# Optimization experiments

Hardware: AMD Instinct MI355X
Metric: run time of the kernel (lower is better)

The kernel has to match this reference:

```python
import jax, jax.numpy as jnp
import numpy as np

HEADS = 8
DIM_KEY = 64


def setup_inputs() -> dict:
    key = jax.random.key(0)
    k1, k2, k3 = jax.random.split(key, 3)
    dim, dim_out = 256, 256
    dim_hidden = HEADS * DIM_KEY  # 512
    img = jax.random.normal(k1, (8, dim, 64, 64), dtype=jnp.float32)
    # 1x1 conv weights stored as [out_ch, in_ch]
    w_qkv = jax.random.normal(k2, (3 * dim_hidden, dim), dtype=jnp.float32) * (dim ** -0.5)
    w_out = jax.random.normal(k3, (dim_out, dim_hidden), dtype=jnp.float32) * (dim_hidden ** -0.5)
    b_out = jnp.zeros((dim_out,), dtype=jnp.float32)
    return {"img": img, "w_qkv": w_qkv, "w_out": w_out, "b_out": b_out}


def reference(img, w_qkv, w_out, b_out):
    b, c, x, y = img.shape
    n = x * y
    # 1x1 conv == channel-mixing GEMM
    qkv = jnp.einsum('oc,bcxy->boxy', w_qkv, img)  # [b, 3*h*dk, x, y]
    q, k, v = jnp.split(qkv, 3, axis=1)
    # 'b (h c) x y -> b h c (x y)'
    reshape = lambda t: t.reshape(b, HEADS, DIM_KEY, n)
    q, k, v = reshape(q), reshape(k), reshape(v)
    k = jax.nn.softmax(k, axis=-1)  # softmax over spatial positions
    context = jnp.einsum('bhdn,bhen->bhde', k, v)      # [b, h, dk, dk]
    content = jnp.einsum('bhde,bhdn->bhen', context, q)  # [b, h, dk, n]
    content = content.reshape(b, HEADS * DIM_KEY, x, y)
    out = jnp.einsum('oc,bcxy->boxy', w_out, content) + b_out[None, :, None, None]
    return out
```

## Files before the change

### kernel.cpp

```cpp
#include <hip/hip_runtime.h>
#include <math.h>
#include <stdint.h>


typedef __attribute__((ext_vector_type(8))) short bf16x8;
typedef __attribute__((ext_vector_type(4))) float f32x4;

#define BATCH 8
#define CIN 256
#define NSP 4096
#define HEADS 8
#define DK 64
#define HID 512
#define OC 256
#define NCH 8
#define NT 4

#define VMCNT(n) asm volatile("s_waitcnt vmcnt(" #n ")" ::: "memory")
#define LGKM0()  asm volatile("s_waitcnt lgkmcnt(0)" ::: "memory")

__device__ __forceinline__ void barrier_fence() {
  asm volatile("" ::: "memory");
  __builtin_amdgcn_s_barrier();
  asm volatile("" ::: "memory");
}

__device__ __forceinline__ void gl16(const void* g, void* l) {
  __builtin_amdgcn_global_load_lds(
      (const __attribute__((address_space(1))) unsigned int*)g,
      (__attribute__((address_space(3))) unsigned int*)l, 16, 0, 0);
}

__device__ __forceinline__ short f2bf(float f) {
  union { float f; uint32_t u; } x; x.f = f;
  uint32_t r = x.u + 0x7fffu + ((x.u >> 16) & 1u);
  return (short)(r >> 16);
}

__device__ __forceinline__ unsigned cvt_pk_bf16(float lo, float hi) {
  unsigned r;
  asm("v_cvt_pk_bf16_f32 %0, %1, %2" : "=v"(r) : "v"(lo), "v"(hi));
  return r;
}

__global__ __launch_bounds__(256) void prep(
    const float* __restrict__ img, const float* __restrict__ w_qkv,
    short* __restrict__ imgT, short* __restrict__ wkv, short* __restrict__ wqT)
{
  __shared__ float t[64][65];
  const int bid = blockIdx.x;
  if (bid < 2048) {
    const int ntile = bid & 63, ctile = (bid >> 6) & 3, b = bid >> 8;
    const float* src = img + ((size_t)b * CIN + ctile * 64) * NSP + ntile * 64;
#pragma unroll
    for (int k = 0; k < 4; ++k) {
      int i = threadIdx.x + k * 256;
      int c = i >> 4, n4 = (i & 15) * 4;
      float4 v = *(const float4*)&src[(size_t)c * NSP + n4];
      t[c][n4 + 0] = v.x; t[c][n4 + 1] = v.y; t[c][n4 + 2] = v.z; t[c][n4 + 3] = v.w;
    }
    __syncthreads();
    short* dst = imgT + ((size_t)b * NSP + ntile * 64) * CIN + ctile * 64;
#pragma unroll
    for (int k = 0; k < 4; ++k) {
      int j = threadIdx.x + k * 256;
      int n = j >> 4, c4 = (j & 15) * 4;
      short r[4] = {f2bf(t[c4 + 0][n]), f2bf(t[c4 + 1][n]),
                    f2bf(t[c4 + 2][n]), f2bf(t[c4 + 3][n])};
      *(uint2*)&dst[(size_t)n * CIN + c4] = *(uint2*)r;
    }
  } else if (bid < 2304) {
    int i = (bid - 2048) * 256 + threadIdx.x;
    const float* src = w_qkv + (size_t)HID * CIN;
    float4 v = ((const float4*)src)[i];
    short r[4] = {f2bf(v.x), f2bf(v.y), f2bf(v.z), f2bf(v.w)};
    *(uint2*)(wkv + (size_t)i * 4) = *(uint2*)r;
  } else {
    const int idx = bid - 2304;
    const int hdt = idx & 7, ct = idx >> 3;
    for (int i = threadIdx.x; i < 4096; i += 256) {
      int r = i >> 6, cc = i & 63;
      t[r][cc] = w_qkv[(size_t)(hdt * 64 + r) * CIN + ct * 64 + cc];
    }
    __syncthreads();
#pragma unroll
    for (int k = 0; k < 4; ++k) {
      int j = threadIdx.x + k * 256;
      int c = j >> 4, h4 = (j & 15) * 4;
      short r[4] = {f2bf(t[h4 + 0][c]), f2bf(t[h4 + 1][c]),
                    f2bf(t[h4 + 2][c]), f2bf(t[h4 + 3][c])};
      *(uint2*)&wqT[(size_t)(ct * 64 + c) * HID + hdt * 64 + h4] = *(uint2*)r;
    }
  }
}

__global__ __launch_bounds__(256, 2) void k1_mfma(
    const short* __restrict__ imgT, const short* __restrict__ wkv,
    float* __restrict__ ctx_part, float* __restrict__ z_part)
{
  const int bi = blockIdx.x;
  const int x = bi & 7, m = bi >> 3;
  const int h = m & 7, g = (m >> 3) * 8 + x;
  const int b = g >> 3, ch = g & 7;

  const int tid = threadIdx.x, w = tid >> 6, l = tid & 63;
  const int l15 = l & 15, l4 = l >> 4;

  __shared__ __align__(16) char sm[81920];
  char* scr = sm + 49152;

  bf16x8 wreg[2][4][2];
#pragma unroll
  for (int tr = 0; tr < 2; ++tr) {
    int row = w * 32 + tr * 16 + l15;
    int gr = (row < 64) ? (h * 64 + row) : (512 + h * 64 + (row - 64));
    const char* base = (const char*)wkv + (size_t)gr * 512;
#pragma unroll
    for (int kq = 0; kq < 4; ++kq)
#pragma unroll
      for (int kk = 0; kk < 2; ++kk)
        wreg[tr][kq][kk] = *(const bf16x8*)(base + kq * 128 + kk * 64 + l4 * 16);
  }
  VMCNT(0);

  const char* ibase = (const char*)imgT + (size_t)b * NSP * 512 + (size_t)ch * 512 * 512;
  const int rowpart = w * 8 + (l >> 3);
  const int colswz = ((l & 7) * 16) ^ (((l >> 3) & 7) << 4);

  auto issue_x = [&](char* buf, int t, int q) {
#pragma unroll
    for (int r = 0; r < 4; ++r) {
      int row = rowpart + r * 32;
      const char* src = ibase + (size_t)(t * 128 + row) * 512 + q * 128 + colswz;
      gl16(src, buf + (size_t)(w * 8 + r * 32) * 128);
    }
  };

  char* p0 = sm; char* p1 = sm + 16384; char* p2 = sm + 32768;
  issue_x(p0, 0, 0);
  issue_x(p1, 0, 1);

  f32x4 acc2[4];
#pragma unroll
  for (int i = 0; i < 4; ++i) acc2[i] = (f32x4){0.f, 0.f, 0.f, 0.f};
  float zacc[2][4];
#pragma unroll
  for (int i = 0; i < 2; ++i)
#pragma unroll
    for (int jj = 0; jj < 4; ++jj) zacc[i][jj] = 0.f;

#define P1Q(BUF, Q)                                                       \
  {                                                                       \
    _Pragma("unroll")                                                     \
    for (int kk = 0; kk < 2; ++kk) {                                      \
      bf16x8 bfr[8];                                                      \
      _Pragma("unroll")                                                   \
      for (int tn = 0; tn < 8; ++tn) {                                    \
        int n = tn * 16 + l15;                                            \
        bfr[tn] = *(bf16x8*)((BUF) + (size_t)n * 128 +                    \
                  ((kk * 64 + l4 * 16) ^ ((n & 7) << 4)));                \
      }                                                                   \
      __builtin_amdgcn_s_setprio(1);                                      \
      _Pragma("unroll")                                                   \
      for (int tr = 0; tr < 2; ++tr)                                      \
        _Pragma("unroll")                                                 \
        for (int tn = 0; tn < 8; ++tn)                                    \
          acc1[tr][tn] = __builtin_amdgcn_mfma_f32_16x16x32_bf16(         \
              wreg[tr][Q][kk], bfr[tn], acc1[tr][tn], 0, 0, 0);           \
      __builtin_amdgcn_s_setprio(0);                                      \
    }                                                                     \
  }

  for (int t = 0; t < NT; ++t) {
    const bool last = (t == NT - 1);
    f32x4 acc1[2][8];
#pragma unroll
    for (int i = 0; i < 2; ++i)
#pragma unroll
      for (int jj = 0; jj < 8; ++jj) acc1[i][jj] = (f32x4){0.f, 0.f, 0.f, 0.f};

    VMCNT(4); barrier_fence();
    issue_x(p2, t, 2);
    P1Q(p0, 0);

    VMCNT(4); barrier_fence();
    issue_x(p0, t, 3);
    P1Q(p1, 1);

    VMCNT(4); barrier_fence();
    if (!last) issue_x(p1, t + 1, 0);
    P1Q(p2, 2);

    if (last) { VMCNT(0); } else { VMCNT(4); }
    barrier_fence();
    if (!last) issue_x(p2, t + 1, 1);
    P1Q(p0, 3);

    {
      char* dst = (w < 2) ? scr : (scr + 16384);
      const int rowb = (w & 1) * 32;
#pragma unroll
      for (int tr = 0; tr < 2; ++tr) {
#pragma unroll
        for (int tn = 0; tn < 8; ++tn) {
          f32x4 vv = acc1[tr][tn];
          float f0 = vv[0], f1 = vv[1], f2 = vv[2], f3 = vv[3];
          if (w < 2) {
            f0 = __expf(f0); f1 = __expf(f1); f2 = __expf(f2); f3 = __expf(f3);
            zacc[tr][0] += f0; zacc[tr][1] += f1;
            zacc[tr][2] += f2; zacc[tr][3] += f3;
          }
          unsigned p01 = cvt_pk_bf16(f0, f1);
          unsigned p23 = cvt_pk_bf16(f2, f3);
          unsigned q01 = (unsigned)__shfl_xor((int)p01, 1, 64);
          unsigned q23 = (unsigned)__shfl_xor((int)p23, 1, 64);
          int nl = tn * 16 + l15;
          int nb = 2 * (nl & ~1);
          int r0 = rowb + tr * 16 + l4 * 4;
          unsigned w0, w1; int rga, rgb;
          if (!(l15 & 1)) {
            w0 = (p01 & 0xffffu) | (q01 << 16);
            w1 = (p01 >> 16) | (q01 & 0xffff0000u);
            rga = 0; rgb = 1;
          } else {
            w0 = (q23 & 0xffffu) | (p23 << 16);
            w1 = (q23 >> 16) | (p23 & 0xffff0000u);
            rga = 2; rgb = 3;
          }
          int rowa = r0 + rga, rowbq = r0 + rgb;
          *(unsigned*)(dst + (size_t)rowa * 256 + (nb ^ ((rowa & 7) << 4))) = w0;
          *(unsigned*)(dst + (size_t)rowbq * 256 + (nb ^ ((rowbq & 7) << 4))) = w1;
        }
      }
    }
    LGKM0(); barrier_fence();
#pragma unroll
    for (int kk = 0; kk < 4; ++kk) {
      int dr = w * 16 + l15;
      bf16x8 a = *(bf16x8*)(scr + (size_t)dr * 256 + ((kk * 64 + l4 * 16) ^ ((dr & 7) << 4)));
      __builtin_amdgcn_s_setprio(1);
#pragma unroll
      for (int te = 0; te < 4; ++te) {
        int er = te * 16 + l15;
        bf16x8 bv = *(bf16x8*)(scr + 16384 + (size_t)er * 256 +
                               ((kk * 64 + l4 * 16) ^ ((er & 7) << 4)));
        acc2[te] = __builtin_amdgcn_mfma_f32_16x16x32_bf16(a, bv, acc2[te], 0, 0, 0);
      }
      __builtin_amdgcn_s_setprio(0);
    }
    { char* tmp = p0; p0 = p1; p1 = p2; p2 = tmp; }
  }

  float* cp = ctx_part + ((size_t)(b * HEADS + h) * NCH + ch) * (DK * DK);
#pragma unroll
  for (int te = 0; te < 4; ++te) {
#pragma unroll
    for (int rg = 0; rg < 4; ++rg) {
      int d = w * 16 + l4 * 4 + rg;
      int e = te * 16 + l15;
      cp[d * 64 + e] = acc2[te][rg];
    }
  }
  if (w < 2) {
#pragma unroll
    for (int tr = 0; tr < 2; ++tr) {
#pragma unroll
      for (int rg = 0; rg < 4; ++rg) {
        float z = zacc[tr][rg];
        z += __shfl_xor(z, 1, 64); z += __shfl_xor(z, 2, 64);
        z += __shfl_xor(z, 4, 64); z += __shfl_xor(z, 8, 64);
        if (l15 == 0) {
          int d = w * 32 + tr * 16 + l4 * 4 + rg;
          z_part[((size_t)(b * HEADS + h) * NCH + ch) * DK + d] = z;
        }
      }
    }
  }
}

__global__ __launch_bounds__(256) void k23_fold(
    const float* __restrict__ ctx_part, const float* __restrict__ z_part,
    const float* __restrict__ w_out, short* __restrict__ M)
{
  const int bid = blockIdx.x;
  const int h = bid & 7, b = (bid >> 3) & 7, ds = bid >> 6;
  const int bh = b * HEADS + h;
  const int d0 = ds * 16;
  __shared__ float cs[16][64];
  __shared__ float zs[16];

  {
    const int idx = threadIdx.x;
    const int dd = idx >> 4, e4 = (idx & 15) * 4;
    float4 s = {0.f, 0.f, 0.f, 0.f};
    for (int chh = 0; chh < NCH; ++chh) {
      const float* p = ctx_part + ((size_t)bh * NCH + chh) * 4096 + (d0 + dd) * 64 + e4;
      float4 v = *(const float4*)p;
      s.x += v.x; s.y += v.y; s.z += v.z; s.w += v.w;
    }
    if ((idx & 15) == 0) {
      float z = 0.f;
      for (int chh = 0; chh < NCH; ++chh)
        z += z_part[((size_t)bh * NCH + chh) * DK + d0 + dd];
      zs[dd] = z;
    }
    cs[dd][e4 + 0] = s.x; cs[dd][e4 + 1] = s.y;
    cs[dd][e4 + 2] = s.z; cs[dd][e4 + 3] = s.w;
  }
  __syncthreads();
  {
    const int idx = threadIdx.x;
    const int dd = idx >> 4, e4 = (idx & 15) * 4;
    float inv = 1.f / zs[dd];
    cs[dd][e4 + 0] *= inv; cs[dd][e4 + 1] *= inv;
    cs[dd][e4 + 2] *= inv; cs[dd][e4 + 3] *= inv;
  }
  __syncthreads();
  const int o = threadIdx.x;
  float4 wr[16];
#pragma unroll
  for (int q = 0; q < 16; ++q)
    wr[q] = *(const float4*)&w_out[(size_t)o * HID + h * DK + q * 4];
#pragma unroll
  for (int dd = 0; dd < 16; ++dd) {
    float a = 0.f;
#pragma unroll
    for (int q = 0; q < 16; ++q) {
      float4 w4 = wr[q];
      a += w4.x * cs[dd][q * 4 + 0] + w4.y * cs[dd][q * 4 + 1]
         + w4.z * cs[dd][q * 4 + 2] + w4.w * cs[dd][q * 4 + 3];
    }
    M[((size_t)b * OC + o) * HID + h * DK + d0 + dd] = f2bf(a);
  }
}

__global__ __launch_bounds__(512) void k3b_mfma(
    const short* __restrict__ M, const short* __restrict__ wqT,
    short* __restrict__ WM)
{
  const int ct = blockIdx.x, b = blockIdx.y;
  const int tid = threadIdx.x, w = tid >> 6, l = tid & 63;
  const int l15 = l & 15, l4 = l >> 4;

  __shared__ __align__(16) char sm3[81920];

  f32x4 acc[4][2];
#pragma unroll
  for (int i = 0; i < 4; ++i)
#pragma unroll
    for (int jj = 0; jj < 2; ++jj) acc[i][jj] = (f32x4){0.f, 0.f, 0.f, 0.f};

  const int srow = tid >> 3, scol = (tid & 7) * 16;
  auto issue = [&](int st, int pb) {
    char* Ab = sm3 + pb * 40960;
    char* Bb = sm3 + 32768 + pb * 40960;
#pragma unroll
    for (int p = 0; p < 4; ++p) {
      int row = p * 64 + srow;
      const char* src = (const char*)M + ((size_t)b * OC + row) * 1024 + st * 128
                        + (scol ^ ((row & 7) << 4));
      gl16(src, Ab + (size_t)(p * 64 + w * 8) * 128);
    }
    {
      int row = srow;
      const char* src = (const char*)wqT + (size_t)(ct * 64 + row) * 1024 + st * 128
                        + (scol ^ ((row & 7) << 4));
      gl16(src, Bb + (size_t)(w * 8) * 128);
    }
  };

  issue(0, 0);
  for (int st = 0; st < 8; ++st) {
    const int pb = st & 1;
    if (st < 7) { issue(st + 1, pb ^ 1); VMCNT(5); } else { VMCNT(0); }
    barrier_fence();
    char* At = sm3 + pb * 40960;
    char* Bt = sm3 + 32768 + pb * 40960;
#pragma unroll
    for (int kk = 0; kk < 2; ++kk) {
      bf16x8 afr[4], bfr[2];
#pragma unroll
      for (int tr = 0; tr < 4; ++tr) {
        int o = (w >> 1) * 64 + tr * 16 + l15;
        afr[tr] = *(bf16x8*)(At + (size_t)o * 128 + ((kk * 64 + l4 * 16) ^ ((o & 7) << 4)));
      }
#pragma unroll
      for (int tn = 0; tn < 2; ++tn) {
        int c = (w & 1) * 32 + tn * 16 + l15;
        bfr[tn] = *(bf16x8*)(Bt + (size_t)c * 128 + ((kk * 64 + l4 * 16) ^ ((c & 7) << 4)));
      }
#pragma unroll
      for (int tr = 0; tr < 4; ++tr)
#pragma unroll
        for (int tn = 0; tn < 2; ++tn)
          acc[tr][tn] = __builtin_amdgcn_mfma_f32_16x16x32_bf16(afr[tr], bfr[tn], acc[tr][tn], 0, 0, 0);
    }
    barrier_fence();
  }
#pragma unroll
  for (int tr = 0; tr < 4; ++tr) {
#pragma unroll
    for (int tn = 0; tn < 2; ++tn) {
#pragma unroll
      for (int rg = 0; rg < 4; ++rg) {
        int o = (w >> 1) * 64 + tr * 16 + l4 * 4 + rg;
        int c = ct * 64 + (w & 1) * 32 + tn * 16 + l15;
        WM[((size_t)b * OC + o) * CIN + c] = f2bf(acc[tr][tn][rg]);
      }
    }
  }
}

__global__ __launch_bounds__(512, 2) void k4_mfma(
    const short* __restrict__ WM, const short* __restrict__ imgT,
    const float* __restrict__ b_out, float* __restrict__ out)
{
  const int bi = blockIdx.x;
  const int b = bi & 7, nt = bi >> 3;
  const int n0 = nt * 64;
  const int tid = threadIdx.x, w = tid >> 6, l = tid & 63;
  const int l15 = l & 15, l4 = l >> 4;

  __shared__ __align__(16) char sm4[24576];
  char* B0 = sm4; char* B1 = sm4 + 8192; char* B2 = sm4 + 16384;

  bf16x8 wreg[2][4][2];
#pragma unroll
  for (int tr = 0; tr < 2; ++tr) {
    int o = w * 32 + tr * 16 + l15;
    const char* base = (const char*)WM + ((size_t)b * OC + o) * 512;
#pragma unroll
    for (int kq = 0; kq < 4; ++kq)
#pragma unroll
      for (int kk = 0; kk < 2; ++kk)
        wreg[tr][kq][kk] = *(const bf16x8*)(base + kq * 128 + kk * 64 + l4 * 16);
  }
  VMCNT(0);

  const char* ibase = (const char*)imgT + ((size_t)b * NSP + n0) * 512;
  const int rowpart = w * 8 + (l >> 3);
  const int colswz = ((l & 7) * 16) ^ (((l >> 3) & 7) << 4);

  auto issue_x = [&](char* buf, int q) {
    const char* src = ibase + (size_t)rowpart * 512 + q * 128 + colswz;
    gl16(src, buf + (size_t)(w * 8) * 128);
  };

  f32x4 acc[2][4];
#pragma unroll
  for (int i = 0; i < 2; ++i)
#pragma unroll
    for (int jj = 0; jj < 4; ++jj) acc[i][jj] = (f32x4){0.f, 0.f, 0.f, 0.f};

#define K4Q(BUF, Q)                                                       \
  {                                                                       \
    _Pragma("unroll")                                                     \
    for (int kk = 0; kk < 2; ++kk) {                                      \
      bf16x8 bfr[4];                                                      \
      _Pragma("unroll")                                                   \
      for (int tn = 0; tn < 4; ++tn) {                                    \
        int n = tn * 16 + l15;                                            \
        bfr[tn] = *(bf16x8*)((BUF) + (size_t)n * 128 +                    \
                  ((kk * 64 + l4 * 16) ^ ((n & 7) << 4)));                \
      }                                                                   \
      __builtin_amdgcn_s_setprio(1);                                      \
      _Pragma("unroll")                                                   \
      for (int tr = 0; tr < 2; ++tr)                                      \
        _Pragma("unroll")                                                 \
        for (int tn = 0; tn < 4; ++tn)                                    \
          acc[tr][tn] = __builtin_amdgcn_mfma_f32_16x16x32_bf16(          \
              wreg[tr][Q][kk], bfr[tn], acc[tr][tn], 0, 0, 0);            \
      __builtin_amdgcn_s_setprio(0);                                      \
    }                                                                     \
  }

  issue_x(B0, 0);
  issue_x(B1, 1);

  VMCNT(1); barrier_fence();
  issue_x(B2, 2);
  K4Q(B0, 0);

  VMCNT(1); barrier_fence();
  issue_x(B0, 3);
  K4Q(B1, 1);

  VMCNT(1); barrier_fence();
  K4Q(B2, 2);

  VMCNT(0); barrier_fence();
  K4Q(B0, 3);

#pragma unroll
  for (int tr = 0; tr < 2; ++tr) {
#pragma unroll
    for (int rg = 0; rg < 4; ++rg) {
      int o = w * 32 + tr * 16 + l4 * 4 + rg;
      float bo = b_out[o];
#pragma unroll
      for (int tn = 0; tn < 4; ++tn) {
        int n = n0 + tn * 16 + l15;
        out[((size_t)b * OC + o) * NSP + n] = acc[tr][tn][rg] + bo;
      }
    }
  }
}

extern "C" void kernel_launch(void* const* d_in, const int* in_sizes, int n_in,
                              void* d_out, int out_size, void* d_ws, size_t ws_size,
                              hipStream_t stream) {
  (void)in_sizes; (void)n_in; (void)out_size; (void)ws_size;
  const float* img   = (const float*)d_in[0];
  const float* w_qkv = (const float*)d_in[1];
  const float* w_out = (const float*)d_in[2];
  const float* b_out = (const float*)d_in[3];
  float* out = (float*)d_out;

  char* ws = (char*)d_ws;
  short* imgT     = (short*)ws;
  short* wkv      = (short*)(ws + 16777216);
  short* wqT      = (short*)(ws + 17301504);
  float* ctx_part = (float*)(ws + 17563648);
  float* z_part   = (float*)(ws + 25952256);
  short* Mbuf     = (short*)(ws + 26083328);
  short* WMbuf    = (short*)(ws + 28180480);

  prep<<<dim3(2336), 256, 0, stream>>>(img, w_qkv, imgT, wkv, wqT);
  k1_mfma<<<dim3(512), 256, 0, stream>>>(imgT, wkv, ctx_part, z_part);
  k23_fold<<<dim3(256), 256, 0, stream>>>(ctx_part, z_part, w_out, Mbuf);
  k3b_mfma<<<dim3(4, 8), 512, 0, stream>>>(Mbuf, wqT, WMbuf);
  k4_mfma<<<dim3(512), 512, 0, stream>>>(WMbuf, imgT, b_out, out);
}
```

Baseline: 82.52 us.

## Replace LDS-staged async tile loads with direct global fragment loads

Removes the global_load_lds triple/double-buffered LDS staging pipelines in k1, k3 and k4. MFMA operand fragments are now read straight from global memory into registers. This frees shared memory and raises k1's occupancy hint to 4 blocks per CU. The cost is losing explicit prefetch overlap and LDS-based reuse across waves, so more redundant global/L2 traffic and exposed load latency become possible.

```diff
diff --git a/kernel.cpp b/kernel.cpp
--- a/kernel.cpp
+++ b/kernel.cpp
@@ -16,19 +16,12 @@
 #define NCH 8
 #define NT 4
 
-#define VMCNT(n) asm volatile("s_waitcnt vmcnt(" #n ")" ::: "memory")
 #define LGKM0()  asm volatile("s_waitcnt lgkmcnt(0)" ::: "memory")
 
 __device__ __forceinline__ void barrier_fence() {
   asm volatile("" ::: "memory");
   __builtin_amdgcn_s_barrier();
   asm volatile("" ::: "memory");
-}
-
-__device__ __forceinline__ void gl16(const void* g, void* l) {
-  __builtin_amdgcn_global_load_lds(
-      (const __attribute__((address_space(1))) unsigned int*)g,
-      (__attribute__((address_space(3))) unsigned int*)l, 16, 0, 0);
 }
 
 __device__ __forceinline__ short f2bf(float f) {
@@ -94,7 +87,7 @@
   }
 }
 
-__global__ __launch_bounds__(256, 2) void k1_mfma(
+__global__ __launch_bounds__(256, 4) void k1_mfma(
     const short* __restrict__ imgT, const short* __restrict__ wkv,
     float* __restrict__ ctx_part, float* __restrict__ z_part)
 {
@@ -106,8 +99,7 @@
   const int tid = threadIdx.x, w = tid >> 6, l = tid & 63;
   const int l15 = l & 15, l4 = l >> 4;
 
-  __shared__ __align__(16) char sm[81920];
-  char* scr = sm + 49152;
+  __shared__ __align__(16) char scr[32768];
 
   bf16x8 wreg[2][4][2];
 #pragma unroll
@@ -121,24 +113,8 @@
       for (int kk = 0; kk < 2; ++kk)
         wreg[tr][kq][kk] = *(const bf16x8*)(base + kq * 128 + kk * 64 + l4 * 16);
   }
-  VMCNT(0);
 
   const char* ibase = (const char*)imgT + (size_t)b * NSP * 512 + (size_t)ch * 512 * 512;
-  const int rowpart = w * 8 + (l >> 3);
-  const int colswz = ((l & 7) * 16) ^ (((l >> 3) & 7) << 4);
-
-  auto issue_x = [&](char* buf, int t, int q) {
-#pragma unroll
-    for (int r = 0; r < 4; ++r) {
-      int row = rowpart + r * 32;
-      const char* src = ibase + (size_t)(t * 128 + row) * 512 + q * 128 + colswz;
-      gl16(src, buf + (size_t)(w * 8 + r * 32) * 128);
-    }
-  };
-
-  char* p0 = sm; char* p1 = sm + 16384; char* p2 = sm + 32768;
-  issue_x(p0, 0, 0);
-  issue_x(p1, 0, 1);
 
   f32x4 acc2[4];
 #pragma unroll
@@ -149,53 +125,35 @@
 #pragma unroll
     for (int jj = 0; jj < 4; ++jj) zacc[i][jj] = 0.f;
 
-#define P1Q(BUF, Q)                                                       \
-  {                                                                       \
-    _Pragma("unroll")                                                     \
-    for (int kk = 0; kk < 2; ++kk) {                                      \
-      bf16x8 bfr[8];                                                      \
-      _Pragma("unroll")                                                   \
-      for (int tn = 0; tn < 8; ++tn) {                                    \
-        int n = tn * 16 + l15;                                            \
-        bfr[tn] = *(bf16x8*)((BUF) + (size_t)n * 128 +                    \
-                  ((kk * 64 + l4 * 16) ^ ((n & 7) << 4)));                \
-      }                                                                   \
-      __builtin_amdgcn_s_setprio(1);                                      \
-      _Pragma("unroll")                                                   \
-      for (int tr = 0; tr < 2; ++tr)                                      \
-        _Pragma("unroll")                                                 \
-        for (int tn = 0; tn < 8; ++tn)                                    \
-          acc1[tr][tn] = __builtin_amdgcn_mfma_f32_16x16x32_bf16(         \
-              wreg[tr][Q][kk], bfr[tn], acc1[tr][tn], 0, 0, 0);           \
-      __builtin_amdgcn_s_setprio(0);                                      \
-    }                                                                     \
-  }
-
   for (int t = 0; t < NT; ++t) {
-    const bool last = (t == NT - 1);
     f32x4 acc1[2][8];
 #pragma unroll
     for (int i = 0; i < 2; ++i)
 #pragma unroll
       for (int jj = 0; jj < 8; ++jj) acc1[i][jj] = (f32x4){0.f, 0.f, 0.f, 0.f};
 
-    VMCNT(4); barrier_fence();
-    issue_x(p2, t, 2);
-    P1Q(p0, 0);
-
-    VMCNT(4); barrier_fence();
-    issue_x(p0, t, 3);
-    P1Q(p1, 1);
-
-    VMCNT(4); barrier_fence();
-    if (!last) issue_x(p1, t + 1, 0);
-    P1Q(p2, 2);
-
-    if (last) { VMCNT(0); } else { VMCNT(4); }
+    const char* tb = ibase + (size_t)t * 128 * 512;
+#pragma unroll
+    for (int q = 0; q < 4; ++q) {
+#pragma unroll
+      for (int kk = 0; kk < 2; ++kk) {
+        bf16x8 bfr[8];
+#pragma unroll
+        for (int tn = 0; tn < 8; ++tn)
+          bfr[tn] = *(const bf16x8*)(tb + (size_t)(tn * 16 + l15) * 512
+                                     + q * 128 + kk * 64 + l4 * 16);
+        __builtin_amdgcn_s_setprio(1);
+#pragma unroll
+        for (int tr = 0; tr < 2; ++tr)
+#pragma unroll
+          for (int tn = 0; tn < 8; ++tn)
+            acc1[tr][tn] = __builtin_amdgcn_mfma_f32_16x16x32_bf16(
+                wreg[tr][q][kk], bfr[tn], acc1[tr][tn], 0, 0, 0);
+        __builtin_amdgcn_s_setprio(0);
+      }
+    }
+
     barrier_fence();
-    if (!last) issue_x(p2, t + 1, 1);
-    P1Q(p0, 3);
-
     {
       char* dst = (w < 2) ? scr : (scr + 16384);
       const int rowb = (w & 1) * 32;
@@ -248,7 +206,6 @@
       }
       __builtin_amdgcn_s_setprio(0);
     }
-    { char* tmp = p0; p0 = p1; p1 = p2; p2 = tmp; }
   }
 
   float* cp = ctx_part + ((size_t)(b * HEADS + h) * NCH + ch) * (DK * DK);
@@ -342,52 +299,29 @@
   const int tid = threadIdx.x, w = tid >> 6, l = tid & 63;
   const int l15 = l & 15, l4 = l >> 4;
 
-  __shared__ __align__(16) char sm3[81920];
-
   f32x4 acc[4][2];
 #pragma unroll
   for (int i = 0; i < 4; ++i)
 #pragma unroll
     for (int jj = 0; jj < 2; ++jj) acc[i][jj] = (f32x4){0.f, 0.f, 0.f, 0.f};
 
-  const int srow = tid >> 3, scol = (tid & 7) * 16;
-  auto issue = [&](int st, int pb) {
-    char* Ab = sm3 + pb * 40960;
-    char* Bb = sm3 + 32768 + pb * 40960;
-#pragma unroll
-    for (int p = 0; p < 4; ++p) {
-      int row = p * 64 + srow;
-      const char* src = (const char*)M + ((size_t)b * OC + row) * 1024 + st * 128
-                        + (scol ^ ((row & 7) << 4));
-      gl16(src, Ab + (size_t)(p * 64 + w * 8) * 128);
-    }
-    {
-      int row = srow;
-      const char* src = (const char*)wqT + (size_t)(ct * 64 + row) * 1024 + st * 128
-                        + (scol ^ ((row & 7) << 4));
-      gl16(src, Bb + (size_t)(w * 8) * 128);
-    }
-  };
-
-  issue(0, 0);
+  const char* Mb = (const char*)M + (size_t)b * OC * 1024;
+  const char* Wb = (const char*)wqT;
+
+#pragma unroll
   for (int st = 0; st < 8; ++st) {
-    const int pb = st & 1;
-    if (st < 7) { issue(st + 1, pb ^ 1); VMCNT(5); } else { VMCNT(0); }
-    barrier_fence();
-    char* At = sm3 + pb * 40960;
-    char* Bt = sm3 + 32768 + pb * 40960;
 #pragma unroll
     for (int kk = 0; kk < 2; ++kk) {
       bf16x8 afr[4], bfr[2];
 #pragma unroll
       for (int tr = 0; tr < 4; ++tr) {
         int o = (w >> 1) * 64 + tr * 16 + l15;
-        afr[tr] = *(bf16x8*)(At + (size_t)o * 128 + ((kk * 64 + l4 * 16) ^ ((o & 7) << 4)));
+        afr[tr] = *(const bf16x8*)(Mb + (size_t)o * 1024 + st * 128 + kk * 64 + l4 * 16);
       }
 #pragma unroll
       for (int tn = 0; tn < 2; ++tn) {
-        int c = (w & 1) * 32 + tn * 16 + l15;
-        bfr[tn] = *(bf16x8*)(Bt + (size_t)c * 128 + ((kk * 64 + l4 * 16) ^ ((c & 7) << 4)));
+        int c = ct * 64 + (w & 1) * 32 + tn * 16 + l15;
+        bfr[tn] = *(const bf16x8*)(Wb + (size_t)c * 1024 + st * 128 + kk * 64 + l4 * 16);
       }
 #pragma unroll
       for (int tr = 0; tr < 4; ++tr)
@@ -395,7 +329,6 @@
         for (int tn = 0; tn < 2; ++tn)
           acc[tr][tn] = __builtin_amdgcn_mfma_f32_16x16x32_bf16(afr[tr], bfr[tn], acc[tr][tn], 0, 0, 0);
     }
-    barrier_fence();
   }
 #pragma unroll
   for (int tr = 0; tr < 4; ++tr) {
@@ -411,7 +344,7 @@
   }
 }
 
-__global__ __launch_bounds__(512, 2) void k4_mfma(
+__global__ __launch_bounds__(512) void k4_mfma(
     const short* __restrict__ WM, const short* __restrict__ imgT,
     const float* __restrict__ b_out, float* __restrict__ out)
 {
@@ -421,9 +354,6 @@
   const int tid = threadIdx.x, w = tid >> 6, l = tid & 63;
   const int l15 = l & 15, l4 = l >> 4;
 
-  __shared__ __align__(16) char sm4[24576];
-  char* B0 = sm4; char* B1 = sm4 + 8192; char* B2 = sm4 + 16384;
-
   bf16x8 wreg[2][4][2];
 #pragma unroll
   for (int tr = 0; tr < 2; ++tr) {
@@ -435,16 +365,8 @@
       for (int kk = 0; kk < 2; ++kk)
         wreg[tr][kq][kk] = *(const bf16x8*)(base + kq * 128 + kk * 64 + l4 * 16);
   }
-  VMCNT(0);
 
   const char* ibase = (const char*)imgT + ((size_t)b * NSP + n0) * 512;
-  const int rowpart = w * 8 + (l >> 3);
-  const int colswz = ((l & 7) * 16) ^ (((l >> 3) & 7) << 4);
-
-  auto issue_x = [&](char* buf, int q) {
-    const char* src = ibase + (size_t)rowpart * 512 + q * 128 + colswz;
-    gl16(src, buf + (size_t)(w * 8) * 128);
-  };
 
   f32x4 acc[2][4];
 #pragma unroll
@@ -452,44 +374,25 @@
 #pragma unroll
     for (int jj = 0; jj < 4; ++jj) acc[i][jj] = (f32x4){0.f, 0.f, 0.f, 0.f};
 
-#define K4Q(BUF, Q)                                                       \
-  {                                                                       \
-    _Pragma("unroll")                                                     \
-    for (int kk = 0; kk < 2; ++kk) {                                      \
-      bf16x8 bfr[4];                                                      \
-      _Pragma("unroll")                                                   \
-      for (int tn = 0; tn < 4; ++tn) {                                    \
-        int n = tn * 16 + l15;                                            \
-        bfr[tn] = *(bf16x8*)((BUF) + (size_t)n * 128 +                    \
-                  ((kk * 64 + l4 * 16) ^ ((n & 7) << 4)));                \
-      }                                                                   \
-      __builtin_amdgcn_s_setprio(1);                                      \
-      _Pragma("unroll")                                                   \
-      for (int tr = 0; tr < 2; ++tr)                                      \
-        _Pragma("unroll")                                                 \
-        for (int tn = 0; tn < 4; ++tn)                                    \
-          acc[tr][tn] = __builtin_amdgcn_mfma_f32_16x16x32_bf16(          \
-              wreg[tr][Q][kk], bfr[tn], acc[tr][tn], 0, 0, 0);            \
-      __builtin_amdgcn_s_setprio(0);                                      \
-    }                                                                     \
-  }
-
-  issue_x(B0, 0);
-  issue_x(B1, 1);
-
-  VMCNT(1); barrier_fence();
-  issue_x(B2, 2);
-  K4Q(B0, 0);
-
-  VMCNT(1); barrier_fence();
-  issue_x(B0, 3);
-  K4Q(B1, 1);
-
-  VMCNT(1); barrier_fence();
-  K4Q(B2, 2);
-
-  VMCNT(0); barrier_fence();
-  K4Q(B0, 3);
+#pragma unroll
+  for (int q = 0; q < 4; ++q) {
+#pragma unroll
+    for (int kk = 0; kk < 2; ++kk) {
+      bf16x8 bfr[4];
+#pragma unroll
+      for (int tn = 0; tn < 4; ++tn)
+        bfr[tn] = *(const bf16x8*)(ibase + (size_t)(tn * 16 + l15) * 512
+                                   + q * 128 + kk * 64 + l4 * 16);
+      __builtin_amdgcn_s_setprio(1);
+#pragma unroll
+      for (int tr = 0; tr < 2; ++tr)
+#pragma unroll
+        for (int tn = 0; tn < 4; ++tn)
+          acc[tr][tn] = __builtin_amdgcn_mfma_f32_16x16x32_bf16(
+              wreg[tr][q][kk], bfr[tn], acc[tr][tn], 0, 0, 0);
+      __builtin_amdgcn_s_setprio(0);
+    }
+  }
 
 #pragma unroll
   for (int tr = 0; tr < 2; ++tr) {
```

After: 181.7 us. +120.1%, slower.
